# Performance work log

Measured on AMD Instinct MI355X. Metric: run time of the kernel, lower is better.

The kernel has to match this reference:

```python
import jax, jax.numpy as jnp
import numpy as np

N, S, D = 4, 8192, 512      # batch, seq, input features
H, HD = 8, 64               # num_heads, attention_dim // num_heads
OUT = 512                   # output_dim
EPS = 1e-6


def setup_inputs() -> dict:
    key = jax.random.key(0)
    ks = jax.random.split(key, 9)
    s_in = 1.0 / np.sqrt(D)
    s_out = 1.0 / np.sqrt(H * HD)
    return {
        "x": jax.random.normal(ks[0], (N, S, D), dtype=jnp.float32),
        "Wq": jax.random.normal(ks[1], (H, D, HD), dtype=jnp.float32) * s_in,
        "bq": jnp.zeros((H, HD), dtype=jnp.float32),
        "Wk": jax.random.normal(ks[2], (H, D, HD), dtype=jnp.float32) * s_in,
        "bk": jnp.zeros((H, HD), dtype=jnp.float32),
        "Wv": jax.random.normal(ks[3], (H, D, HD), dtype=jnp.float32) * s_in,
        "bv": jnp.zeros((H, HD), dtype=jnp.float32),
        "Wo": jax.random.normal(ks[4], (H * HD, OUT), dtype=jnp.float32) * s_out,
        "bo": jnp.zeros((OUT,), dtype=jnp.float32),
    }


def reference(x, Wq, bq, Wk, bk, Wv, bv, Wo, bo):
    fmap = lambda t: jax.nn.elu(t) + 1.0  # elu+1 feature map
    # per-head projections, vectorized over heads: [n,H,s,hd]
    Q = fmap(jnp.einsum('nsd,hdk->nhsk', x, Wq) + bq[None, :, None, :])
    K = fmap(jnp.einsum('nsd,hdk->nhsk', x, Wk) + bk[None, :, None, :])
    V = jnp.einsum('nsd,hdk->nhsk', x, Wv) + bv[None, :, None, :]
    # KV = sum_s K*V  (einsum 'nsh,nsh->nh' in the original, per head)
    KV = jnp.sum(K * V, axis=2)           # [n,H,hd]
    Ksum = jnp.sum(K, axis=2)             # [n,H,hd]
    Z = 1.0 / (Q * Ksum[:, :, None, :] + EPS)
    O = Q * KV[:, :, None, :] * Z         # [n,H,s,hd]
    # concat heads along last axis (head-major ordering matches the python loop)
    O = jnp.transpose(O, (0, 2, 1, 3)).reshape(N, S, H * HD)
    return jax.nn.gelu(O @ Wo + bo)       # flax nn.gelu default (approximate)
```

## Files before the change

kernel.cpp:

```cpp
#include <hip/hip_runtime.h>

typedef __bf16 bf16x8 __attribute__((ext_vector_type(8)));
typedef float  f32x4  __attribute__((ext_vector_type(4)));

#define LDS_AS(p)  ((__attribute__((address_space(3))) void*)(p))
#define GLB_AS(p)  ((const __attribute__((address_space(1))) void*)(p))

__device__ __forceinline__ unsigned short f2bf(float f){
  unsigned u = __float_as_uint(f);
  return (unsigned short)((u + 0x7fffu + ((u >> 16) & 1u)) >> 16);
}

__global__ void prep_kernel(const float* __restrict__ Wk, const float* __restrict__ Wv,
                            unsigned short* __restrict__ Wt, float* __restrict__ accg){
  int i = blockIdx.x * 256 + threadIdx.x;
  if (i < 6144) accg[i] = 0.f;
  int f  = i >> 9, d = i & 511;
  int gf = f >> 4, t = f & 15;
  int c  = (gf >> 1) * 16 + t;
  const float* W = (gf & 1) ? Wv : Wk;
  int h = c >> 6, hd = c & 63;
  Wt[i] = f2bf(W[(h * 512 + d) * 64 + hd]);
}

__global__ __launch_bounds__(256) void kv_kernel(const float* __restrict__ x,
    const unsigned short* __restrict__ Wt, const float* __restrict__ bk,
    const float* __restrict__ bv, float* __restrict__ accg){
  __shared__ __align__(16) unsigned short As[128 * 64];
  __shared__ __align__(16) unsigned short Bs[128 * 64];

  int bid = blockIdx.x;
  int wg  = (bid & 7) * 256 + (bid >> 3);
  int panel = wg >> 3;
  int bcol  = wg & 7;
  int row0  = panel << 7;
  int n     = panel >> 6;
  int tid = threadIdx.x;
  int l = tid & 63, w = tid >> 6;
  int wr = w >> 1, wc = w & 1;

  const f32x4 vz = {0.f, 0.f, 0.f, 0.f};
  f32x4 accv[4][4];
  #pragma unroll
  for (int m = 0; m < 4; ++m)
    #pragma unroll
    for (int q = 0; q < 4; ++q) accv[m][q] = vz;

  int rA = w * 32 + (l >> 3);
  int cc = l & 7;
  const float* xg = x + (size_t)(row0 + rA) * 512 + cc * 8;

  float4 fA[4][2];
  #pragma unroll
  for (int j = 0; j < 4; ++j){
    const float* g = xg + (size_t)j * 8 * 512;
    fA[j][0] = *(const float4*)g;
    fA[j][1] = *(const float4*)(g + 4);
  }

  for (int kt = 0; kt < 8; ++kt){
    if (kt) __syncthreads();
    #pragma unroll
    for (int j = 0; j < 4; ++j){
      int r  = rA + 8 * j;
      int sw = ((r >> 1) & 7) << 4;
      float4 f0 = fA[j][0], f1 = fA[j][1];
      bf16x8 v;
      v[0]=(__bf16)f0.x; v[1]=(__bf16)f0.y; v[2]=(__bf16)f0.z; v[3]=(__bf16)f0.w;
      v[4]=(__bf16)f1.x; v[5]=(__bf16)f1.y; v[6]=(__bf16)f1.z; v[7]=(__bf16)f1.w;
      *(bf16x8*)((char*)As + r * 128 + ((cc * 16) ^ sw)) = v;
    }
    #pragma unroll
    for (int i = 0; i < 4; ++i){
      int L   = (w * 4 + i) * 1024 + l * 16;
      int col = L >> 7;
      int s   = L & 127;
      int sb  = kt * 128 + (s ^ (((col >> 1) & 7) << 4));
      const char* g = (const char*)Wt + (size_t)(bcol * 128 + col) * 1024 + sb;
      char* lb = (char*)Bs + (size_t)(w * 4 + i) * 1024;
      __builtin_amdgcn_global_load_lds(GLB_AS(g), LDS_AS(lb), 16, 0, 0);
    }
    __syncthreads();

    if (kt < 7){
      const float* gk = xg + (kt + 1) * 64;
      #pragma unroll
      for (int j = 0; j < 4; ++j){
        const float* g = gk + (size_t)j * 8 * 512;
        fA[j][0] = *(const float4*)g;
        fA[j][1] = *(const float4*)(g + 4);
      }
    }

    #pragma unroll
    for (int kk = 0; kk < 2; ++kk){
      bf16x8 aF[4], bF[4];
      int kb = kk * 64 + (l >> 4) * 16;
      #pragma unroll
      for (int m = 0; m < 4; ++m){
        int row = wr * 64 + m * 16 + (l & 15);
        aF[m] = *(const bf16x8*)((const char*)As + row * 128 + (kb ^ (((row >> 1) & 7) << 4)));
      }
      #pragma unroll
      for (int q = 0; q < 4; ++q){
        int col = wc * 64 + q * 16 + (l & 15);
        bF[q] = *(const bf16x8*)((const char*)Bs + col * 128 + (kb ^ (((col >> 1) & 7) << 4)));
      }
      #pragma unroll
      for (int m = 0; m < 4; ++m)
        #pragma unroll
        for (int q = 0; q < 4; ++q)
          accv[m][q] = __builtin_amdgcn_mfma_f32_16x16x32_bf16(aF[m], bF[q], accv[m][q], 0, 0, 0);
    }
  }

  #pragma unroll
  for (int p = 0; p < 2; ++p){
    int q = p * 2;
    int c = (bcol * 4 + wc * 2 + p) * 16 + (l & 15);
    float bkc = bk[c], bvc = bv[c];
    float sKV = 0.f, sK = 0.f;
    #pragma unroll
    for (int m = 0; m < 4; ++m)
      #pragma unroll
      for (int r = 0; r < 4; ++r){
        float kp  = accv[m][q][r] + bkc;
        float kvv = kp > 0.f ? kp + 1.f : __expf(kp);
        sKV += kvv * (accv[m][q + 1][r] + bvc);
        sK  += kvv;
      }
    sKV += __shfl_xor(sKV, 16); sKV += __shfl_xor(sKV, 32);
    sK  += __shfl_xor(sK , 16); sK  += __shfl_xor(sK , 32);
    if ((l >> 4) == 0){
      atomicAdd(&accg[n * 1024 + c],       sKV);
      atomicAdd(&accg[n * 1024 + 512 + c], sK);
    }
  }
}

__global__ void fin1_kernel(const float* __restrict__ accg, const float* __restrict__ Wo,
                            float* __restrict__ pre){
  int b = blockIdx.x;
  int n = b >> 6, cb = b & 63;
  int t = threadIdx.x;
  __shared__ float ov[8];
  if (t < 8){ int c = cb * 8 + t; ov[t] = accg[n * 1024 + c] / accg[n * 1024 + 512 + c]; }
  __syncthreads();
  float s0 = 0.f, s1 = 0.f;
  #pragma unroll
  for (int j = 0; j < 8; ++j){
    int c = cb * 8 + j;
    s0 += ov[j] * Wo[c * 512 + t];
    s1 += ov[j] * Wo[c * 512 + 256 + t];
  }
  atomicAdd(&pre[n * 512 + t],       s0);
  atomicAdd(&pre[n * 512 + 256 + t], s1);
}

__global__ void fin2_kernel(const float* __restrict__ pre, const float* __restrict__ bo,
                            float* __restrict__ rows){
  int i = blockIdx.x * 512 + threadIdx.x;
  float s = pre[i] + bo[i & 511];
  float t = 0.7978845608028654f * (s + 0.044715f * s * s * s);
  rows[i] = 0.5f * s * (1.f + tanhf(t));
}

__global__ void bcast_kernel(const float* __restrict__ rows, float4* __restrict__ out){
  int i = blockIdx.x * 256 + threadIdx.x;
  int n  = i >> 20;
  int o4 = i & 127;
  out[i] = *(const float4*)(rows + n * 512 + o4 * 4);
}

extern "C" void kernel_launch(void* const* d_in, const int* in_sizes, int n_in,
                              void* d_out, int out_size, void* d_ws, size_t ws_size,
                              hipStream_t stream){
  const float* x  = (const float*)d_in[0];
  const float* Wk = (const float*)d_in[3];
  const float* bk = (const float*)d_in[4];
  const float* Wv = (const float*)d_in[5];
  const float* bv = (const float*)d_in[6];
  const float* Wo = (const float*)d_in[7];
  const float* bo = (const float*)d_in[8];
  float* out = (float*)d_out;

  char* ws = (char*)d_ws;
  unsigned short* Wt = (unsigned short*)ws;
  float* accg = (float*)(ws + (1 << 20));
  float* pre  = (float*)(ws + (1 << 20) + 16384);
  float* rows = (float*)(ws + (1 << 20) + 24576);

  prep_kernel<<<2048, 256, 0, stream>>>(Wk, Wv, Wt, accg);
  kv_kernel  <<<2048, 256, 0, stream>>>(x, Wt, bk, bv, accg);
  fin1_kernel<<<256, 256, 0, stream>>>(accg, Wo, pre);
  fin2_kernel<<<4, 512, 0, stream>>>(pre, bo, rows);
  bcast_kernel<<<16384, 256, 0, stream>>>(rows, (float4*)out);
}
```

Baseline: 178.7 us.

## Load B fragments directly to registers and fuse GELU into broadcast

The kv kernel no longer stages the Wk/Wv bf16 tile in shared memory. Each lane loads its MFMA B fragments straight from global memory into registers and prefetches the next k-step's fragments. The x tile is now converted to bf16 at load time, and the k-loop is fully unrolled. Separately, the GELU finalisation kernel is fused into the broadcast kernel, which computes each row in shared memory and writes 8 float4 per thread, removing one launch. The trade-off is more register pressure and redundant global loads of B across the two row-warps, in exchange for fewer LDS writes and barriers.

Measured after the change: 209.7 us. 17.3% more time.

```diff
diff --git a/kernel.cpp b/kernel.cpp
--- a/kernel.cpp
+++ b/kernel.cpp
@@ -2,9 +2,6 @@
 
 typedef __bf16 bf16x8 __attribute__((ext_vector_type(8)));
 typedef float  f32x4  __attribute__((ext_vector_type(4)));
-
-#define LDS_AS(p)  ((__attribute__((address_space(3))) void*)(p))
-#define GLB_AS(p)  ((const __attribute__((address_space(1))) void*)(p))
 
 __device__ __forceinline__ unsigned short f2bf(float f){
   unsigned u = __float_as_uint(f);
@@ -27,7 +24,6 @@
     const unsigned short* __restrict__ Wt, const float* __restrict__ bk,
     const float* __restrict__ bv, float* __restrict__ accg){
   __shared__ __align__(16) unsigned short As[128 * 64];
-  __shared__ __align__(16) unsigned short Bs[128 * 64];
 
   int bid = blockIdx.x;
   int wg  = (bid & 7) * 256 + (bid >> 3);
@@ -50,35 +46,34 @@
   int cc = l & 7;
   const float* xg = x + (size_t)(row0 + rA) * 512 + cc * 8;
 
-  float4 fA[4][2];
+  const unsigned short* Bg = Wt + (size_t)(bcol * 128 + wc * 64 + (l & 15)) * 512 + (l >> 4) * 8;
+
+  bf16x8 bfA[4];
   #pragma unroll
   for (int j = 0; j < 4; ++j){
     const float* g = xg + (size_t)j * 8 * 512;
-    fA[j][0] = *(const float4*)g;
-    fA[j][1] = *(const float4*)(g + 4);
-  }
-
+    float4 f0 = *(const float4*)g;
+    float4 f1 = *(const float4*)(g + 4);
+    bf16x8 v;
+    v[0]=(__bf16)f0.x; v[1]=(__bf16)f0.y; v[2]=(__bf16)f0.z; v[3]=(__bf16)f0.w;
+    v[4]=(__bf16)f1.x; v[5]=(__bf16)f1.y; v[6]=(__bf16)f1.z; v[7]=(__bf16)f1.w;
+    bfA[j] = v;
+  }
+  bf16x8 bCur[2][4];
+  #pragma unroll
+  for (int kk = 0; kk < 2; ++kk)
+    #pragma unroll
+    for (int q = 0; q < 4; ++q)
+      bCur[kk][q] = *(const bf16x8*)(Bg + q * 8192 + kk * 32);
+
+  #pragma unroll
   for (int kt = 0; kt < 8; ++kt){
     if (kt) __syncthreads();
     #pragma unroll
     for (int j = 0; j < 4; ++j){
       int r  = rA + 8 * j;
       int sw = ((r >> 1) & 7) << 4;
-      float4 f0 = fA[j][0], f1 = fA[j][1];
-      bf16x8 v;
-      v[0]=(__bf16)f0.x; v[1]=(__bf16)f0.y; v[2]=(__bf16)f0.z; v[3]=(__bf16)f0.w;
-      v[4]=(__bf16)f1.x; v[5]=(__bf16)f1.y; v[6]=(__bf16)f1.z; v[7]=(__bf16)f1.w;
-      *(bf16x8*)((char*)As + r * 128 + ((cc * 16) ^ sw)) = v;
-    }
-    #pragma unroll
-    for (int i = 0; i < 4; ++i){
-      int L   = (w * 4 + i) * 1024 + l * 16;
-      int col = L >> 7;
-      int s   = L & 127;
-      int sb  = kt * 128 + (s ^ (((col >> 1) & 7) << 4));
-      const char* g = (const char*)Wt + (size_t)(bcol * 128 + col) * 1024 + sb;
-      char* lb = (char*)Bs + (size_t)(w * 4 + i) * 1024;
-      __builtin_amdgcn_global_load_lds(GLB_AS(g), LDS_AS(lb), 16, 0, 0);
+      *(bf16x8*)((char*)As + r * 128 + ((cc * 16) ^ sw)) = bfA[j];
     }
     __syncthreads();
 
@@ -87,14 +82,18 @@
       #pragma unroll
       for (int j = 0; j < 4; ++j){
         const float* g = gk + (size_t)j * 8 * 512;
-        fA[j][0] = *(const float4*)g;
-        fA[j][1] = *(const float4*)(g + 4);
+        float4 f0 = *(const float4*)g;
+        float4 f1 = *(const float4*)(g + 4);
+        bf16x8 v;
+        v[0]=(__bf16)f0.x; v[1]=(__bf16)f0.y; v[2]=(__bf16)f0.z; v[3]=(__bf16)f0.w;
+        v[4]=(__bf16)f1.x; v[5]=(__bf16)f1.y; v[6]=(__bf16)f1.z; v[7]=(__bf16)f1.w;
+        bfA[j] = v;
       }
     }
 
     #pragma unroll
     for (int kk = 0; kk < 2; ++kk){
-      bf16x8 aF[4], bF[4];
+      bf16x8 aF[4];
       int kb = kk * 64 + (l >> 4) * 16;
       #pragma unroll
       for (int m = 0; m < 4; ++m){
@@ -102,15 +101,16 @@
         aF[m] = *(const bf16x8*)((const char*)As + row * 128 + (kb ^ (((row >> 1) & 7) << 4)));
       }
       #pragma unroll
-      for (int q = 0; q < 4; ++q){
-        int col = wc * 64 + q * 16 + (l & 15);
-        bF[q] = *(const bf16x8*)((const char*)Bs + col * 128 + (kb ^ (((col >> 1) & 7) << 4)));
-      }
-      #pragma unroll
       for (int m = 0; m < 4; ++m)
         #pragma unroll
         for (int q = 0; q < 4; ++q)
-          accv[m][q] = __builtin_amdgcn_mfma_f32_16x16x32_bf16(aF[m], bF[q], accv[m][q], 0, 0, 0);
+          accv[m][q] = __builtin_amdgcn_mfma_f32_16x16x32_bf16(aF[m], bCur[kk][q], accv[m][q], 0, 0, 0);
+      if (kt < 7){
+        const unsigned short* bg = Bg + (kt + 1) * 64 + kk * 32;
+        #pragma unroll
+        for (int q = 0; q < 4; ++q)
+          bCur[kk][q] = *(const bf16x8*)(bg + q * 8192);
+      }
     }
   }
 
@@ -157,19 +157,25 @@
   atomicAdd(&pre[n * 512 + 256 + t], s1);
 }
 
-__global__ void fin2_kernel(const float* __restrict__ pre, const float* __restrict__ bo,
-                            float* __restrict__ rows){
-  int i = blockIdx.x * 512 + threadIdx.x;
-  float s = pre[i] + bo[i & 511];
-  float t = 0.7978845608028654f * (s + 0.044715f * s * s * s);
-  rows[i] = 0.5f * s * (1.f + tanhf(t));
-}
-
-__global__ void bcast_kernel(const float* __restrict__ rows, float4* __restrict__ out){
-  int i = blockIdx.x * 256 + threadIdx.x;
-  int n  = i >> 20;
-  int o4 = i & 127;
-  out[i] = *(const float4*)(rows + n * 512 + o4 * 4);
+__global__ void bcast_kernel(const float* __restrict__ pre, const float* __restrict__ bo,
+                             float4* __restrict__ out){
+  __shared__ float row[512];
+  int bid = blockIdx.x;
+  int n = bid >> 9, bc = bid & 511;
+  int t = threadIdx.x;
+  #pragma unroll
+  for (int j = 0; j < 2; ++j){
+    int o = t + j * 256;
+    float s = pre[n * 512 + o] + bo[o];
+    float u = 0.7978845608028654f * (s + 0.044715f * s * s * s);
+    row[o] = 0.5f * s * (1.f + tanhf(u));
+  }
+  __syncthreads();
+  float4 v = ((const float4*)row)[t & 127];
+  float4* dst = out + ((size_t)n << 20) + bc * 2048;
+  #pragma unroll
+  for (int it = 0; it < 8; ++it)
+    dst[it * 256 + t] = v;
 }
 
 extern "C" void kernel_launch(void* const* d_in, const int* in_sizes, int n_in,
@@ -188,11 +194,9 @@
   unsigned short* Wt = (unsigned short*)ws;
   float* accg = (float*)(ws + (1 << 20));
   float* pre  = (float*)(ws + (1 << 20) + 16384);
-  float* rows = (float*)(ws + (1 << 20) + 24576);
-
-  prep_kernel<<<2048, 256, 0, stream>>>(Wk, Wv, Wt, accg);
-  kv_kernel  <<<2048, 256, 0, stream>>>(x, Wt, bk, bv, accg);
-  fin1_kernel<<<256, 256, 0, stream>>>(accg, Wo, pre);
-  fin2_kernel<<<4, 512, 0, stream>>>(pre, bo, rows);
-  bcast_kernel<<<16384, 256, 0, stream>>>(rows, (float4*)out);
-}
+
+  prep_kernel <<<2048, 256, 0, stream>>>(Wk, Wv, Wt, accg);
+  kv_kernel   <<<2048, 256, 0, stream>>>(x, Wt, bk, bv, accg);
+  fin1_kernel <<<256, 256, 0, stream>>>(accg, Wo, pre);
+  bcast_kernel<<<2048, 256, 0, stream>>>(pre, bo, (float4*)out);
+}
```

## Widen KV GEMM tile and fuse output projection into last-block epilogue

Applied to the files above, without the earlier changes.

Each block now computes a 128x256 tile of the K/V projection instead of 128x128. This halves the number of blocks and the number of times each x panel is loaded and converted to bf16. The separate fin1/fin2 kernels are removed; an atomic counter picks the last finishing block, which computes KV/Ksum, the Wo projection for all batches, the bias and GELU serially. The broadcast kernel is rewritten so each block writes a contiguous 2048-float4 chunk from an LDS-cached row. The trade-offs are higher register and LDS use per block and a serial 512x512x4 tail on a single workgroup.

After: 241.0 us. +34.8%, slower.

```diff
diff --git a/kernel.cpp b/kernel.cpp
--- a/kernel.cpp
+++ b/kernel.cpp
@@ -23,28 +23,30 @@
   Wt[i] = f2bf(W[(h * 512 + d) * 64 + hd]);
 }
 
-__global__ __launch_bounds__(256) void kv_kernel(const float* __restrict__ x,
+__global__ __launch_bounds__(256, 2) void kv_kernel(const float* __restrict__ x,
     const unsigned short* __restrict__ Wt, const float* __restrict__ bk,
-    const float* __restrict__ bv, float* __restrict__ accg){
+    const float* __restrict__ bv, float* __restrict__ accg,
+    const float* __restrict__ Wo, const float* __restrict__ bo,
+    float* __restrict__ rows, int* __restrict__ cnt){
   __shared__ __align__(16) unsigned short As[128 * 64];
-  __shared__ __align__(16) unsigned short Bs[128 * 64];
+  __shared__ __align__(16) unsigned short Bs[256 * 64];
+  __shared__ int lastBlk;
 
   int bid = blockIdx.x;
-  int wg  = (bid & 7) * 256 + (bid >> 3);
-  int panel = wg >> 3;
-  int bcol  = wg & 7;
-  int row0  = panel << 7;
-  int n     = panel >> 6;
+  int wg  = (bid & 7) * 128 + (bid >> 3);
+  int rowp = wg >> 2, colp = wg & 3;
+  int row0 = rowp << 7;
+  int n    = rowp >> 6;
   int tid = threadIdx.x;
   int l = tid & 63, w = tid >> 6;
   int wr = w >> 1, wc = w & 1;
 
   const f32x4 vz = {0.f, 0.f, 0.f, 0.f};
-  f32x4 accv[4][4];
+  f32x4 acc[4][8];
   #pragma unroll
   for (int m = 0; m < 4; ++m)
     #pragma unroll
-    for (int q = 0; q < 4; ++q) accv[m][q] = vz;
+    for (int q = 0; q < 8; ++q) acc[m][q] = vz;
 
   int rA = w * 32 + (l >> 3);
   int cc = l & 7;
@@ -71,13 +73,13 @@
       *(bf16x8*)((char*)As + r * 128 + ((cc * 16) ^ sw)) = v;
     }
     #pragma unroll
-    for (int i = 0; i < 4; ++i){
-      int L   = (w * 4 + i) * 1024 + l * 16;
+    for (int i = 0; i < 8; ++i){
+      int L   = (w * 8 + i) * 1024 + l * 16;
       int col = L >> 7;
       int s   = L & 127;
       int sb  = kt * 128 + (s ^ (((col >> 1) & 7) << 4));
-      const char* g = (const char*)Wt + (size_t)(bcol * 128 + col) * 1024 + sb;
-      char* lb = (char*)Bs + (size_t)(w * 4 + i) * 1024;
+      const char* g = (const char*)Wt + (size_t)(colp * 256 + col) * 1024 + sb;
+      char* lb = (char*)Bs + (size_t)(w * 8 + i) * 1024;
       __builtin_amdgcn_global_load_lds(GLB_AS(g), LDS_AS(lb), 16, 0, 0);
     }
     __syncthreads();
@@ -94,7 +96,7 @@
 
     #pragma unroll
     for (int kk = 0; kk < 2; ++kk){
-      bf16x8 aF[4], bF[4];
+      bf16x8 aF[4], bF[8];
       int kb = kk * 64 + (l >> 4) * 16;
       #pragma unroll
       for (int m = 0; m < 4; ++m){
@@ -102,31 +104,30 @@
         aF[m] = *(const bf16x8*)((const char*)As + row * 128 + (kb ^ (((row >> 1) & 7) << 4)));
       }
       #pragma unroll
-      for (int q = 0; q < 4; ++q){
-        int col = wc * 64 + q * 16 + (l & 15);
+      for (int q = 0; q < 8; ++q){
+        int col = wc * 128 + q * 16 + (l & 15);
         bF[q] = *(const bf16x8*)((const char*)Bs + col * 128 + (kb ^ (((col >> 1) & 7) << 4)));
       }
       #pragma unroll
       for (int m = 0; m < 4; ++m)
         #pragma unroll
-        for (int q = 0; q < 4; ++q)
-          accv[m][q] = __builtin_amdgcn_mfma_f32_16x16x32_bf16(aF[m], bF[q], accv[m][q], 0, 0, 0);
-    }
-  }
-
-  #pragma unroll
-  for (int p = 0; p < 2; ++p){
-    int q = p * 2;
-    int c = (bcol * 4 + wc * 2 + p) * 16 + (l & 15);
+        for (int q = 0; q < 8; ++q)
+          acc[m][q] = __builtin_amdgcn_mfma_f32_16x16x32_bf16(aF[m], bF[q], acc[m][q], 0, 0, 0);
+    }
+  }
+
+  #pragma unroll
+  for (int p = 0; p < 4; ++p){
+    int c = (colp * 8 + wc * 4 + p) * 16 + (l & 15);
     float bkc = bk[c], bvc = bv[c];
     float sKV = 0.f, sK = 0.f;
     #pragma unroll
     for (int m = 0; m < 4; ++m)
       #pragma unroll
       for (int r = 0; r < 4; ++r){
-        float kp  = accv[m][q][r] + bkc;
+        float kp  = acc[m][2 * p][r] + bkc;
         float kvv = kp > 0.f ? kp + 1.f : __expf(kp);
-        sKV += kvv * (accv[m][q + 1][r] + bvc);
+        sKV += kvv * (acc[m][2 * p + 1][r] + bvc);
         sK  += kvv;
       }
     sKV += __shfl_xor(sKV, 16); sKV += __shfl_xor(sKV, 32);
@@ -136,40 +137,58 @@
       atomicAdd(&accg[n * 1024 + 512 + c], sK);
     }
   }
-}
-
-__global__ void fin1_kernel(const float* __restrict__ accg, const float* __restrict__ Wo,
-                            float* __restrict__ pre){
-  int b = blockIdx.x;
-  int n = b >> 6, cb = b & 63;
+
+  __syncthreads();
+  if (tid == 0){
+    __threadfence();
+    int prev = __hip_atomic_fetch_add(cnt, 1, __ATOMIC_ACQ_REL, __HIP_MEMORY_SCOPE_AGENT);
+    lastBlk = (prev == (int)gridDim.x - 1);
+  }
+  __syncthreads();
+  if (!lastBlk) return;
+
+  float* ov = (float*)As;
+  #pragma unroll
+  for (int n2 = 0; n2 < 4; ++n2)
+    #pragma unroll
+    for (int j = 0; j < 2; ++j){
+      int c = tid + j * 256;
+      ov[n2 * 512 + c] = accg[n2 * 1024 + c] / accg[n2 * 1024 + 512 + c];
+    }
+  __syncthreads();
+  float s[4][2] = {{0.f,0.f},{0.f,0.f},{0.f,0.f},{0.f,0.f}};
+  for (int c = 0; c < 512; ++c){
+    float w0 = Wo[c * 512 + tid], w1 = Wo[c * 512 + 256 + tid];
+    #pragma unroll
+    for (int n2 = 0; n2 < 4; ++n2){
+      float o = ov[n2 * 512 + c];
+      s[n2][0] += o * w0;
+      s[n2][1] += o * w1;
+    }
+  }
+  #pragma unroll
+  for (int n2 = 0; n2 < 4; ++n2)
+    #pragma unroll
+    for (int j = 0; j < 2; ++j){
+      int o = tid + j * 256;
+      float v = s[n2][j] + bo[o];
+      float u = 0.7978845608028654f * (v + 0.044715f * v * v * v);
+      rows[n2 * 512 + o] = 0.5f * v * (1.f + tanhf(u));
+    }
+}
+
+__global__ void bcast_kernel(const float* __restrict__ rows, float4* __restrict__ out){
+  __shared__ float4 row4[128];
+  int bid = blockIdx.x;
+  int n = bid >> 9, bc = bid & 511;
   int t = threadIdx.x;
-  __shared__ float ov[8];
-  if (t < 8){ int c = cb * 8 + t; ov[t] = accg[n * 1024 + c] / accg[n * 1024 + 512 + c]; }
-  __syncthreads();
-  float s0 = 0.f, s1 = 0.f;
-  #pragma unroll
-  for (int j = 0; j < 8; ++j){
-    int c = cb * 8 + j;
-    s0 += ov[j] * Wo[c * 512 + t];
-    s1 += ov[j] * Wo[c * 512 + 256 + t];
-  }
-  atomicAdd(&pre[n * 512 + t],       s0);
-  atomicAdd(&pre[n * 512 + 256 + t], s1);
-}
-
-__global__ void fin2_kernel(const float* __restrict__ pre, const float* __restrict__ bo,
-                            float* __restrict__ rows){
-  int i = blockIdx.x * 512 + threadIdx.x;
-  float s = pre[i] + bo[i & 511];
-  float t = 0.7978845608028654f * (s + 0.044715f * s * s * s);
-  rows[i] = 0.5f * s * (1.f + tanhf(t));
-}
-
-__global__ void bcast_kernel(const float* __restrict__ rows, float4* __restrict__ out){
-  int i = blockIdx.x * 256 + threadIdx.x;
-  int n  = i >> 20;
-  int o4 = i & 127;
-  out[i] = *(const float4*)(rows + n * 512 + o4 * 4);
+  if (t < 128) row4[t] = ((const float4*)(rows + n * 512))[t];
+  __syncthreads();
+  float4 v = row4[t & 127];
+  float4* dst = out + ((size_t)n << 20) + bc * 2048;
+  #pragma unroll
+  for (int it = 0; it < 8; ++it)
+    dst[it * 256 + t] = v;
 }
 
 extern "C" void kernel_launch(void* const* d_in, const int* in_sizes, int n_in,
@@ -187,12 +206,10 @@
   char* ws = (char*)d_ws;
   unsigned short* Wt = (unsigned short*)ws;
   float* accg = (float*)(ws + (1 << 20));
-  float* pre  = (float*)(ws + (1 << 20) + 16384);
-  float* rows = (float*)(ws + (1 << 20) + 24576);
-
-  prep_kernel<<<2048, 256, 0, stream>>>(Wk, Wv, Wt, accg);
-  kv_kernel  <<<2048, 256, 0, stream>>>(x, Wt, bk, bv, accg);
-  fin1_kernel<<<256, 256, 0, stream>>>(accg, Wo, pre);
-  fin2_kernel<<<4, 512, 0, stream>>>(pre, bo, rows);
-  bcast_kernel<<<16384, 256, 0, stream>>>(rows, (float4*)out);
-}
+  int*   cnt  = (int*)(ws + (1 << 20) + 16384);
+  float* rows = (float*)(ws + (1 << 20) + 20480);
+
+  prep_kernel <<<2048, 256, 0, stream>>>(Wk, Wv, Wt, accg);
+  kv_kernel   <<<1024, 256, 0, stream>>>(x, Wt, bk, bv, accg, Wo, bo, rows, cnt);
+  bcast_kernel<<<2048, 256, 0, stream>>>(rows, (float4*)out);
+}
```
